# Optimization experiments

Measured on AMD Instinct MI355X. Metric: run time of the kernel, lower is better.

Reference implementation:

```python
import jax, jax.numpy as jnp
import numpy as np

B, T, A, OBS = 4096, 32, 4, 115
H, K, ACT = 64, 8, 19
FEAT = 4 + 3 + 4 * A          # 23 structured features
IN_DIM = FEAT + ACT * A       # 99 with action one-hots


def setup_inputs() -> dict:
    key = jax.random.key(0)
    ks = jax.random.split(key, 16)
    s = lambda *sh: 1.0 / np.sqrt(sh[-1])
    inp = {
        "obs_seq": jax.random.normal(ks[0], (B, T, A, OBS), jnp.float32),
        "action_seq": jax.random.randint(ks[1], (B, T, A), 0, ACT, jnp.int32),
        # feature_proj: Linear(IN_DIM->H) + LayerNorm(H)
        "proj_W": jax.random.normal(ks[2], (H, IN_DIM), jnp.float32) * s(H, IN_DIM),
        "proj_b": jnp.zeros((H,), jnp.float32),
        "ln_g": jnp.ones((H,), jnp.float32),
        "ln_b": jnp.zeros((H,), jnp.float32),
        # 2-layer GRU
        "Wih0": jax.random.normal(ks[3], (3 * H, H), jnp.float32) * s(1, H),
        "Whh0": jax.random.normal(ks[4], (3 * H, H), jnp.float32) * s(1, H),
        "bih0": jnp.zeros((3 * H,), jnp.float32),
        "bhh0": jnp.zeros((3 * H,), jnp.float32),
        "Wih1": jax.random.normal(ks[5], (3 * H, H), jnp.float32) * s(1, H),
        "Whh1": jax.random.normal(ks[6], (3 * H, H), jnp.float32) * s(1, H),
        "bih1": jnp.zeros((3 * H,), jnp.float32),
        "bhh1": jnp.zeros((3 * H,), jnp.float32),
        # classifier MLP
        "cls_W1": jax.random.normal(ks[7], (H, H), jnp.float32) * s(H, H),
        "cls_b1": jnp.zeros((H,), jnp.float32),
        "cls_W2": jax.random.normal(ks[8], (K, H), jnp.float32) * s(K, H),
        "cls_b2": jnp.zeros((K,), jnp.float32),
    }
    return inp


def _extract_features(obs_seq, action_seq):
    b, t, a = obs_seq.shape[:3]
    # ball position from player 0's obs, and its finite-difference velocity
    ball_pos = obs_seq[:, :, 0, 88:90]                       # [B,T,2]
    ball_vel = jnp.concatenate(
        [jnp.zeros_like(ball_pos[:, :1]), ball_pos[:, 1:] - ball_pos[:, :-1]], axis=1)
    pos = obs_seq[..., 0:2]                                   # [B,T,A,2]
    pos_flat = pos.reshape(b, t, a * 2)
    centroid = pos.mean(axis=2)                               # [B,T,2]
    spread = jnp.sqrt(((pos - centroid[:, :, None]) ** 2).sum(-1).mean(2, keepdims=True) + 1e-6)
    # closest-teammate relative position: vectorized argmin over pairwise dists
    diff = pos[:, :, :, None, :] - pos[:, :, None, :, :]      # [B,T,A,A,2]
    d2 = (diff ** 2).sum(-1)                                  # [B,T,A,A]
    d2 = jnp.where(jnp.eye(a, dtype=bool), jnp.inf, d2)       # exclude self
    idx = jnp.argmin(d2, axis=-1)                             # [B,T,A]
    nearest = jnp.take_along_axis(pos, idx[..., None], axis=2)  # [B,T,A,2]
    closest_rel = (nearest - pos).reshape(b, t, a * 2)
    onehot = jax.nn.one_hot(action_seq, ACT, dtype=jnp.float32).reshape(b, t, a * ACT)
    return jnp.concatenate(
        [ball_pos, ball_vel, pos_flat, centroid, spread, closest_rel, onehot], axis=-1)


def _gru_layer(x_tbh, Wih, Whh, bih, bhh):
    h0 = jnp.zeros((x_tbh.shape[1], Whh.shape[1]), x_tbh.dtype)

    def step(h, x):
        gi = x @ Wih.T + bih
        gh = h @ Whh.T + bhh
        ir, iz, inn = jnp.split(gi, 3, axis=-1)
        hr, hz, hn = jnp.split(gh, 3, axis=-1)
        r = jax.nn.sigmoid(ir + hr)
        z = jax.nn.sigmoid(iz + hz)
        n = jnp.tanh(inn + r * hn)
        h_new = (1.0 - z) * n + z * h
        return h_new, h_new

    h_last, ys = jax.lax.scan(step, h0, x_tbh)
    return ys, h_last


def reference(obs_seq, action_seq, proj_W, proj_b, ln_g, ln_b,
              Wih0, Whh0, bih0, bhh0, Wih1, Whh1, bih1, bhh1,
              cls_W1, cls_b1, cls_W2, cls_b2):
    feats = _extract_features(obs_seq, action_seq)            # [B,T,99]
    x = feats @ proj_W.T + proj_b                             # [B,T,H]
    mu = x.mean(-1, keepdims=True)
    var = x.var(-1, keepdims=True)
    x = (x - mu) * jax.lax.rsqrt(var + 1e-5) * ln_g + ln_b
    x = jax.nn.relu(x)
    x = jnp.swapaxes(x, 0, 1)                                 # [T,B,H]
    ys0, _ = _gru_layer(x, Wih0, Whh0, bih0, bhh0)
    _, h_last = _gru_layer(ys0, Wih1, Whh1, bih1, bhh1)       # [B,H]
    hid = jax.nn.relu(h_last @ cls_W1.T + cls_b1)
    logits = hid @ cls_W2.T + cls_b2                          # [B,K]
    return logits
```

## Files before the change

kernel.cpp:

```cpp
#include <hip/hip_runtime.h>

#define B_ 4096
#define T_ 32
#define A_ 4
#define OBS_ 115
#define H_ 64
#define IN_DIM_ 99
#define ACT_ 19
#define NBT (B_*T_)

typedef _Float16 f16;
typedef _Float16 f16x8 __attribute__((ext_vector_type(8)));
typedef float f32x4 __attribute__((ext_vector_type(4)));

static __device__ __forceinline__ float sigmoid_f(float x) {
    return 1.f / (1.f + __expf(-x));
}
static __device__ __forceinline__ float tanh_f(float x) {
    return 1.f - 2.f / (1.f + __expf(2.f * x));
}
static __device__ __forceinline__ f32x4 mfma16(f16x8 a, f16x8 b, f32x4 c) {
    return __builtin_amdgcn_mfma_f32_16x16x32_f16(a, b, c, 0, 0, 0);
}

__global__ __launch_bounds__(256) void k0_transpose(const float* __restrict__ W,
                                                    float* __restrict__ WT) {
    int idx = blockIdx.x * 256 + threadIdx.x;
    if (idx < IN_DIM_ * H_) {
        int i = idx >> 6, h = idx & 63;
        WT[idx] = W[h * IN_DIM_ + i];
    }
}

__global__ __launch_bounds__(256) void k1_feats(const float* __restrict__ obs,
                                                float* __restrict__ feats) {
    __shared__ float fl[256 * 25];
    int tid = threadIdx.x;
    int n = blockIdx.x * 256 + tid;
    const float* o = obs + (size_t)n * (A_ * OBS_);

    float px[A_], py[A_];
#pragma unroll
    for (int a = 0; a < A_; a++) { px[a] = o[a * OBS_]; py[a] = o[a * OBS_ + 1]; }
    float bx = o[88], by = o[89];
    int t = n & (T_ - 1);
    float pbx = bx, pby = by;
    if (t > 0) { pbx = o[88 - A_ * OBS_]; pby = o[89 - A_ * OBS_]; }

    float cx = (px[0] + px[1] + px[2] + px[3]) * 0.25f;
    float cy = (py[0] + py[1] + py[2] + py[3]) * 0.25f;
    float sp = 0.f;
#pragma unroll
    for (int a = 0; a < A_; a++) { float dx = px[a] - cx, dy = py[a] - cy; sp += dx * dx + dy * dy; }
    sp = sqrtf(sp * 0.25f + 1e-6f);

    float crx[A_], cry[A_];
#pragma unroll
    for (int i = 0; i < A_; i++) {
        float best = 3.4e38f; int bj = 0;
#pragma unroll
        for (int j = 0; j < A_; j++) {
            if (j == i) continue;
            float dx = px[i] - px[j], dy = py[i] - py[j];
            float d2 = dx * dx + dy * dy;
            if (d2 < best) { best = d2; bj = j; }
        }
        crx[i] = px[bj] - px[i]; cry[i] = py[bj] - py[i];
    }

    float* f = &fl[tid * 25];
    f[0] = bx; f[1] = by; f[2] = bx - pbx; f[3] = by - pby;
#pragma unroll
    for (int a = 0; a < A_; a++) { f[4 + 2 * a] = px[a]; f[5 + 2 * a] = py[a]; }
    f[12] = cx; f[13] = cy; f[14] = sp;
#pragma unroll
    for (int a = 0; a < A_; a++) { f[15 + 2 * a] = crx[a]; f[16 + 2 * a] = cry[a]; }
    __syncthreads();

    size_t base = (size_t)blockIdx.x * 256 * 32;
    for (int k = tid; k < 256 * 32; k += 256) {
        int i = k & 31, r = k >> 5;
        feats[base + k] = (i < 23) ? fl[r * 25 + i] : 0.f;
    }
}

__global__ __launch_bounds__(256) void k1b_proj(const float* __restrict__ feats,
                                                const int* __restrict__ act,
                                                const float* __restrict__ WT,
                                                const float* __restrict__ pb,
                                                const float* __restrict__ lng,
                                                const float* __restrict__ lnb,
                                                f16* __restrict__ xout) {
    int lane = threadIdx.x & 63;
    int wv = __builtin_amdgcn_readfirstlane(threadIdx.x >> 6);
    int b = blockIdx.x * 4 + wv;

    float wc[23];
#pragma unroll
    for (int i = 0; i < 23; i++) wc[i] = WT[i * 64 + lane];
    float pbv = pb[lane], g = lng[lane], bb = lnb[lane];

    for (int t = 0; t < T_; t++) {
        int bt = b * T_ + t;
        const float* fp = feats + (size_t)bt * 32;
        float v = pbv;
#pragma unroll
        for (int i = 0; i < 23; i++) v += fp[i] * wc[i];
#pragma unroll
        for (int a = 0; a < A_; a++) {
            int ai = act[bt * A_ + a];
            v += WT[(23 + a * ACT_ + ai) * 64 + lane];
        }
        float s = v, ss = v * v;
#pragma unroll
        for (int m = 1; m < 64; m <<= 1) {
            s += __shfl_xor(s, m, 64);
            ss += __shfl_xor(ss, m, 64);
        }
        float mean = s * (1.f / 64.f);
        float var = ss * (1.f / 64.f) - mean * mean;
        float xn = (v - mean) * rsqrtf(var + 1e-5f) * g + bb;
        xn = fmaxf(xn, 0.f);
        xout[((size_t)t * B_ + b) * 64 + lane] = (f16)xn;
    }
}

__global__ __launch_bounds__(256, 1) void k2_gru(
        const f16* __restrict__ x,
        const float* __restrict__ Wih0, const float* __restrict__ Whh0,
        const float* __restrict__ bih0, const float* __restrict__ bhh0,
        const float* __restrict__ Wih1, const float* __restrict__ Whh1,
        const float* __restrict__ bih1, const float* __restrict__ bhh1,
        const float* __restrict__ W1, const float* __restrict__ b1,
        const float* __restrict__ W2, const float* __restrict__ b2,
        float* __restrict__ out) {
    __shared__ __align__(16) f16 hbuf[2][2][16 * 72];
    int tid = threadIdx.x;
    int lane = tid & 63;
    int wv = __builtin_amdgcn_readfirstlane(tid >> 6);
    int c = lane & 15, q = lane >> 4;
    int S = wv * 16;
    int rowbase = blockIdx.x * 16;

    for (int k = tid; k < 2 * 2 * 16 * 72; k += 256) ((f16*)hbuf)[k] = (f16)0.f;

    auto ldw = [&](const float* W, int row0, int kcol) -> f16x8 {
        const float* p = W + (size_t)(row0 + c) * 64 + kcol + q * 8;
        f32x4 w0 = *(const f32x4*)p;
        f32x4 w1 = *(const f32x4*)(p + 4);
        f16x8 r;
        r[0] = (f16)w0[0]; r[1] = (f16)w0[1]; r[2] = (f16)w0[2]; r[3] = (f16)w0[3];
        r[4] = (f16)w1[0]; r[5] = (f16)w1[1]; r[6] = (f16)w1[2]; r[7] = (f16)w1[3];
        return r;
    };

    f16x8 wih0[3][2], whh0[3][2], wih1[3][2], whh1[3][2];
#pragma unroll
    for (int g = 0; g < 3; g++)
#pragma unroll
        for (int kf = 0; kf < 2; kf++) {
            wih0[g][kf] = ldw(Wih0, g * 64 + S, kf * 32);
            whh0[g][kf] = ldw(Whh0, g * 64 + S, kf * 32);
            wih1[g][kf] = ldw(Wih1, g * 64 + S, kf * 32);
            whh1[g][kf] = ldw(Whh1, g * 64 + S, kf * 32);
        }

    float br0 = bih0[S + c] + bhh0[S + c];
    float bz0 = bih0[64 + S + c] + bhh0[64 + S + c];
    float bi0 = bih0[128 + S + c];
    float bh0 = bhh0[128 + S + c];
    float br1 = bih1[S + c] + bhh1[S + c];
    float bz1 = bih1[64 + S + c] + bhh1[64 + S + c];
    float bi1 = bih1[128 + S + c];
    float bh1 = bhh1[128 + S + c];
    f32x4 vbr0 = {br0, br0, br0, br0}, vbz0 = {bz0, bz0, bz0, bz0};
    f32x4 vbi0 = {bi0, bi0, bi0, bi0}, vbh0 = {bh0, bh0, bh0, bh0};
    f32x4 vbr1 = {br1, br1, br1, br1}, vbz1 = {bz1, bz1, bz1, bz1};
    f32x4 vbi1 = {bi1, bi1, bi1, bi1}, vbh1 = {bh1, bh1, bh1, bh1};

    f32x4 h0c = {0.f, 0.f, 0.f, 0.f}, h1c = {0.f, 0.f, 0.f, 0.f};

    auto ldx = [&](int t, int kf) -> f16x8 {
        return *(const f16x8*)(x + ((size_t)t * B_ + rowbase + c) * 64 + kf * 32 + q * 8);
    };

    __syncthreads();

    int p = 0;
    f16x8 xa0 = ldx(0, 0), xa1 = ldx(0, 1);
    f16x8 xn0 = xa0, xn1 = xa1;

    for (int i = 0; i <= T_; i++) {
        if (i + 1 < T_) { xn0 = ldx(i + 1, 0); xn1 = ldx(i + 1, 1); }

        f16x8 a00 = *(const f16x8*)&hbuf[0][p][c * 72 + q * 8];
        f16x8 a01 = *(const f16x8*)&hbuf[0][p][c * 72 + 32 + q * 8];

        if (i < T_) {
            f32x4 r = vbr0, z = vbz0, in = vbi0, hn = vbh0;
            r = mfma16(a00, whh0[0][0], r); r = mfma16(a01, whh0[0][1], r);
            r = mfma16(xa0, wih0[0][0], r); r = mfma16(xa1, wih0[0][1], r);
            z = mfma16(a00, whh0[1][0], z); z = mfma16(a01, whh0[1][1], z);
            z = mfma16(xa0, wih0[1][0], z); z = mfma16(xa1, wih0[1][1], z);
            in = mfma16(xa0, wih0[2][0], in); in = mfma16(xa1, wih0[2][1], in);
            hn = mfma16(a00, whh0[2][0], hn); hn = mfma16(a01, whh0[2][1], hn);
#pragma unroll
            for (int rr = 0; rr < 4; rr++) {
                float rg = sigmoid_f(r[rr]);
                float zg = sigmoid_f(z[rr]);
                float ng = tanh_f(in[rr] + rg * hn[rr]);
                h0c[rr] = ng + zg * (h0c[rr] - ng);
            }
        }
        if (i > 0) {
            f16x8 a10 = *(const f16x8*)&hbuf[1][p][c * 72 + q * 8];
            f16x8 a11 = *(const f16x8*)&hbuf[1][p][c * 72 + 32 + q * 8];
            f32x4 r = vbr1, z = vbz1, in = vbi1, hn = vbh1;
            r = mfma16(a10, whh1[0][0], r); r = mfma16(a11, whh1[0][1], r);
            r = mfma16(a00, wih1[0][0], r); r = mfma16(a01, wih1[0][1], r);
            z = mfma16(a10, whh1[1][0], z); z = mfma16(a11, whh1[1][1], z);
            z = mfma16(a00, wih1[1][0], z); z = mfma16(a01, wih1[1][1], z);
            in = mfma16(a00, wih1[2][0], in); in = mfma16(a01, wih1[2][1], in);
            hn = mfma16(a10, whh1[2][0], hn); hn = mfma16(a11, whh1[2][1], hn);
#pragma unroll
            for (int rr = 0; rr < 4; rr++) {
                float rg = sigmoid_f(r[rr]);
                float zg = sigmoid_f(z[rr]);
                float ng = tanh_f(in[rr] + rg * hn[rr]);
                h1c[rr] = ng + zg * (h1c[rr] - ng);
            }
        }
#pragma unroll
        for (int rr = 0; rr < 4; rr++) {
            hbuf[0][p ^ 1][(q * 4 + rr) * 72 + S + c] = (f16)h0c[rr];
            hbuf[1][p ^ 1][(q * 4 + rr) * 72 + S + c] = (f16)h1c[rr];
        }
        __syncthreads();
        p ^= 1;
        xa0 = xn0; xa1 = xn1;
    }

    f16x8 ha0 = *(const f16x8*)&hbuf[1][p][c * 72 + q * 8];
    f16x8 ha1 = *(const f16x8*)&hbuf[1][p][c * 72 + 32 + q * 8];
    f16x8 w1f0 = ldw(W1, S, 0), w1f1 = ldw(W1, S, 32);
    float bw1 = b1[S + c];
    f32x4 hid = {bw1, bw1, bw1, bw1};
    hid = mfma16(ha0, w1f0, hid);
    hid = mfma16(ha1, w1f1, hid);
#pragma unroll
    for (int rr = 0; rr < 4; rr++) {
        float hv = fmaxf(hid[rr], 0.f);
        hbuf[0][p ^ 1][(q * 4 + rr) * 72 + S + c] = (f16)hv;
    }
    __syncthreads();
    if (wv == 0) {
        f16x8 ga0 = *(const f16x8*)&hbuf[0][p ^ 1][c * 72 + q * 8];
        f16x8 ga1 = *(const f16x8*)&hbuf[0][p ^ 1][c * 72 + 32 + q * 8];
        f16x8 w2f0 = {}, w2f1 = {};
        float bo = 0.f;
        if (c < 8) {
            w2f0 = ldw(W2, 0, 0);
            w2f1 = ldw(W2, 0, 32);
            bo = b2[c];
        }
        f32x4 lg = {bo, bo, bo, bo};
        lg = mfma16(ga0, w2f0, lg);
        lg = mfma16(ga1, w2f1, lg);
        if (c < 8) {
#pragma unroll
            for (int rr = 0; rr < 4; rr++)
                out[(size_t)(rowbase + q * 4 + rr) * 8 + c] = lg[rr];
        }
    }
}

extern "C" void kernel_launch(void* const* d_in, const int* in_sizes, int n_in,
                              void* d_out, int out_size, void* d_ws, size_t ws_size,
                              hipStream_t stream) {
    const float* obs  = (const float*)d_in[0];
    const int*   act  = (const int*)d_in[1];
    const float* projW = (const float*)d_in[2];
    const float* projb = (const float*)d_in[3];
    const float* lng  = (const float*)d_in[4];
    const float* lnb  = (const float*)d_in[5];
    const float* Wih0 = (const float*)d_in[6];
    const float* Whh0 = (const float*)d_in[7];
    const float* bih0 = (const float*)d_in[8];
    const float* bhh0 = (const float*)d_in[9];
    const float* Wih1 = (const float*)d_in[10];
    const float* Whh1 = (const float*)d_in[11];
    const float* bih1 = (const float*)d_in[12];
    const float* bhh1 = (const float*)d_in[13];
    const float* W1   = (const float*)d_in[14];
    const float* b1   = (const float*)d_in[15];
    const float* W2   = (const float*)d_in[16];
    const float* b2   = (const float*)d_in[17];
    float* out = (float*)d_out;

    char* ws = (char*)d_ws;
    float* WT    = (float*)ws;
    float* feats = (float*)(ws + 32768);
    f16*   xw    = (f16*)(ws + 32768 + (size_t)NBT * 32 * 4);

    k0_transpose<<<25, 256, 0, stream>>>(projW, WT);
    k1_feats<<<NBT / 256, 256, 0, stream>>>(obs, feats);
    k1b_proj<<<B_ / 4, 256, 0, stream>>>(feats, act, WT, projb, lng, lnb, xw);
    k2_gru<<<B_ / 16, 256, 0, stream>>>(xw, Wih0, Whh0, bih0, bhh0,
                                        Wih1, Whh1, bih1, bhh1,
                                        W1, b1, W2, b2, out);
}
```

Measured before the change: 404.8 us.

## Fuse feature extraction with projection and halve GRU rows per block

Merges the feature-extraction and projection/LayerNorm kernels into one, keeping per-timestep features and action indices in shared memory so the intermediate feats buffer never goes through global memory. Separately, the GRU kernel now processes 8 batch rows per block instead of 16 and allows 2 blocks per CU, which doubles the grid to fill more CUs on the latency-bound recurrence. The cost is that the 16-row MFMA tiles are half wasted: the extra rows are clamped duplicates whose results are discarded.

```diff
diff --git a/kernel.cpp b/kernel.cpp
--- a/kernel.cpp
+++ b/kernel.cpp
@@ -32,83 +32,78 @@
     }
 }
 
-__global__ __launch_bounds__(256) void k1_feats(const float* __restrict__ obs,
-                                                float* __restrict__ feats) {
-    __shared__ float fl[256 * 25];
-    int tid = threadIdx.x;
-    int n = blockIdx.x * 256 + tid;
-    const float* o = obs + (size_t)n * (A_ * OBS_);
-
-    float px[A_], py[A_];
-#pragma unroll
-    for (int a = 0; a < A_; a++) { px[a] = o[a * OBS_]; py[a] = o[a * OBS_ + 1]; }
-    float bx = o[88], by = o[89];
-    int t = n & (T_ - 1);
-    float pbx = bx, pby = by;
-    if (t > 0) { pbx = o[88 - A_ * OBS_]; pby = o[89 - A_ * OBS_]; }
-
-    float cx = (px[0] + px[1] + px[2] + px[3]) * 0.25f;
-    float cy = (py[0] + py[1] + py[2] + py[3]) * 0.25f;
-    float sp = 0.f;
-#pragma unroll
-    for (int a = 0; a < A_; a++) { float dx = px[a] - cx, dy = py[a] - cy; sp += dx * dx + dy * dy; }
-    sp = sqrtf(sp * 0.25f + 1e-6f);
-
-    float crx[A_], cry[A_];
-#pragma unroll
-    for (int i = 0; i < A_; i++) {
-        float best = 3.4e38f; int bj = 0;
-#pragma unroll
-        for (int j = 0; j < A_; j++) {
-            if (j == i) continue;
-            float dx = px[i] - px[j], dy = py[i] - py[j];
-            float d2 = dx * dx + dy * dy;
-            if (d2 < best) { best = d2; bj = j; }
-        }
-        crx[i] = px[bj] - px[i]; cry[i] = py[bj] - py[i];
-    }
-
-    float* f = &fl[tid * 25];
-    f[0] = bx; f[1] = by; f[2] = bx - pbx; f[3] = by - pby;
-#pragma unroll
-    for (int a = 0; a < A_; a++) { f[4 + 2 * a] = px[a]; f[5 + 2 * a] = py[a]; }
-    f[12] = cx; f[13] = cy; f[14] = sp;
-#pragma unroll
-    for (int a = 0; a < A_; a++) { f[15 + 2 * a] = crx[a]; f[16 + 2 * a] = cry[a]; }
-    __syncthreads();
-
-    size_t base = (size_t)blockIdx.x * 256 * 32;
-    for (int k = tid; k < 256 * 32; k += 256) {
-        int i = k & 31, r = k >> 5;
-        feats[base + k] = (i < 23) ? fl[r * 25 + i] : 0.f;
-    }
-}
-
-__global__ __launch_bounds__(256) void k1b_proj(const float* __restrict__ feats,
+__global__ __launch_bounds__(256) void k1_fused(const float* __restrict__ obs,
                                                 const int* __restrict__ act,
                                                 const float* __restrict__ WT,
                                                 const float* __restrict__ pb,
                                                 const float* __restrict__ lng,
                                                 const float* __restrict__ lnb,
                                                 f16* __restrict__ xout) {
-    int lane = threadIdx.x & 63;
-    int wv = __builtin_amdgcn_readfirstlane(threadIdx.x >> 6);
-    int b = blockIdx.x * 4 + wv;
-
+    __shared__ float fl[256 * 25];
+    __shared__ int al[256 * 5];
+    int tid = threadIdx.x;
+    int n = blockIdx.x * 256 + tid;
+    const float* o = obs + (size_t)n * (A_ * OBS_);
+
+    float px[A_], py[A_];
+#pragma unroll
+    for (int a = 0; a < A_; a++) { px[a] = o[a * OBS_]; py[a] = o[a * OBS_ + 1]; }
+    float bx = o[88], by = o[89];
+    int t0 = n & (T_ - 1);
+    float pbx = bx, pby = by;
+    if (t0 > 0) { pbx = o[88 - A_ * OBS_]; pby = o[89 - A_ * OBS_]; }
+
+    float cx = (px[0] + px[1] + px[2] + px[3]) * 0.25f;
+    float cy = (py[0] + py[1] + py[2] + py[3]) * 0.25f;
+    float sp = 0.f;
+#pragma unroll
+    for (int a = 0; a < A_; a++) { float dx = px[a] - cx, dy = py[a] - cy; sp += dx * dx + dy * dy; }
+    sp = sqrtf(sp * 0.25f + 1e-6f);
+
+    float crx[A_], cry[A_];
+#pragma unroll
+    for (int i = 0; i < A_; i++) {
+        float best = 3.4e38f; int bj = 0;
+#pragma unroll
+        for (int j = 0; j < A_; j++) {
+            if (j == i) continue;
+            float dx = px[i] - px[j], dy = py[i] - py[j];
+            float d2 = dx * dx + dy * dy;
+            if (d2 < best) { best = d2; bj = j; }
+        }
+        crx[i] = px[bj] - px[i]; cry[i] = py[bj] - py[i];
+    }
+
+    float* f = &fl[tid * 25];
+    f[0] = bx; f[1] = by; f[2] = bx - pbx; f[3] = by - pby;
+#pragma unroll
+    for (int a = 0; a < A_; a++) { f[4 + 2 * a] = px[a]; f[5 + 2 * a] = py[a]; }
+    f[12] = cx; f[13] = cy; f[14] = sp;
+#pragma unroll
+    for (int a = 0; a < A_; a++) { f[15 + 2 * a] = crx[a]; f[16 + 2 * a] = cry[a]; }
+#pragma unroll
+    for (int a = 0; a < A_; a++) al[tid * 5 + a] = act[n * A_ + a];
+    __syncthreads();
+
+    int lane = tid & 63;
+    int wv = __builtin_amdgcn_readfirstlane(tid >> 6);
     float wc[23];
 #pragma unroll
     for (int i = 0; i < 23; i++) wc[i] = WT[i * 64 + lane];
     float pbv = pb[lane], g = lng[lane], bb = lnb[lane];
-
-    for (int t = 0; t < T_; t++) {
-        int bt = b * T_ + t;
-        const float* fp = feats + (size_t)bt * 32;
+    int b0 = blockIdx.x * 8 + wv * 2;
+
+    for (int it = 0; it < 64; it++) {
+        int lb = wv * 64 + it;
+        int b = b0 + (it >> 5);
+        int t = it & 31;
+        const float* fp = &fl[lb * 25];
         float v = pbv;
 #pragma unroll
         for (int i = 0; i < 23; i++) v += fp[i] * wc[i];
 #pragma unroll
         for (int a = 0; a < A_; a++) {
-            int ai = act[bt * A_ + a];
+            int ai = al[lb * 5 + a];
             v += WT[(23 + a * ACT_ + ai) * 64 + lane];
         }
         float s = v, ss = v * v;
@@ -125,7 +120,8 @@
     }
 }
 
-__global__ __launch_bounds__(256, 1) void k2_gru(
+#define ROWS_ 8
+__global__ __launch_bounds__(256, 2) void k2_gru(
         const f16* __restrict__ x,
         const float* __restrict__ Wih0, const float* __restrict__ Whh0,
         const float* __restrict__ bih0, const float* __restrict__ bhh0,
@@ -140,7 +136,7 @@
     int wv = __builtin_amdgcn_readfirstlane(tid >> 6);
     int c = lane & 15, q = lane >> 4;
     int S = wv * 16;
-    int rowbase = blockIdx.x * 16;
+    int rowbase = blockIdx.x * ROWS_;
 
     for (int k = tid; k < 2 * 2 * 16 * 72; k += 256) ((f16*)hbuf)[k] = (f16)0.f;
 
@@ -181,7 +177,9 @@
     f32x4 h0c = {0.f, 0.f, 0.f, 0.f}, h1c = {0.f, 0.f, 0.f, 0.f};
 
     auto ldx = [&](int t, int kf) -> f16x8 {
-        return *(const f16x8*)(x + ((size_t)t * B_ + rowbase + c) * 64 + kf * 32 + q * 8);
+        int row = rowbase + c;
+        if (row >= B_) row = B_ - 1;
+        return *(const f16x8*)(x + ((size_t)t * B_ + row) * 64 + kf * 32 + q * 8);
     };
 
     __syncthreads();
@@ -268,8 +266,11 @@
         lg = mfma16(ga1, w2f1, lg);
         if (c < 8) {
 #pragma unroll
-            for (int rr = 0; rr < 4; rr++)
-                out[(size_t)(rowbase + q * 4 + rr) * 8 + c] = lg[rr];
+            for (int rr = 0; rr < 4; rr++) {
+                int row = q * 4 + rr;
+                if (row < ROWS_)
+                    out[(size_t)(rowbase + row) * 8 + c] = lg[rr];
+            }
         }
     }
 }
@@ -298,14 +299,12 @@
     float* out = (float*)d_out;
 
     char* ws = (char*)d_ws;
-    float* WT    = (float*)ws;
-    float* feats = (float*)(ws + 32768);
-    f16*   xw    = (f16*)(ws + 32768 + (size_t)NBT * 32 * 4);
+    float* WT = (float*)ws;
+    f16*   xw = (f16*)(ws + 32768);
 
     k0_transpose<<<25, 256, 0, stream>>>(projW, WT);
-    k1_feats<<<NBT / 256, 256, 0, stream>>>(obs, feats);
-    k1b_proj<<<B_ / 4, 256, 0, stream>>>(feats, act, WT, projb, lng, lnb, xw);
-    k2_gru<<<B_ / 16, 256, 0, stream>>>(xw, Wih0, Whh0, bih0, bhh0,
-                                        Wih1, Whh1, bih1, bhh1,
-                                        W1, b1, W2, b2, out);
-}
+    k1_fused<<<NBT / 256, 256, 0, stream>>>(obs, act, WT, projb, lng, lnb, xw);
+    k2_gru<<<B_ / ROWS_, 256, 0, stream>>>(xw, Wih0, Whh0, bih0, bhh0,
+                                           Wih1, Whh1, bih1, bhh1,
+                                           W1, b1, W2, b2, out);
+}
```

After: 424.5 us. 1.05x slower.
